# Optimization experiments

Hardware: AMD Instinct MI355X
Metric: run time of the kernel (lower is better)

## Reference

```python
import jax, jax.numpy as jnp
import numpy as np

N = 100_000      # nodes
E = 1_600_000    # directed edges
D_IN, D_H, D_OUT = 128, 128, 1


def setup_inputs() -> dict:
    key = jax.random.key(0)
    ks = jax.random.split(key, 6)
    x = jax.random.normal(ks[0], (N, D_IN), dtype=jnp.float32)
    edge_index = jax.random.randint(ks[1], (2, E), 0, N, dtype=jnp.int32)
    # GCNConv params (glorot-ish scale)
    W1 = jax.random.normal(ks[2], (D_IN, D_H), dtype=jnp.float32) / np.sqrt(D_IN)
    b1 = jnp.zeros((D_H,), dtype=jnp.float32)
    W2 = jax.random.normal(ks[3], (D_H, D_OUT), dtype=jnp.float32) / np.sqrt(D_H)
    b2 = jnp.zeros((D_OUT,), dtype=jnp.float32)
    return {"x": x, "edge_index": edge_index, "W1": W1, "b1": b1, "W2": W2, "b2": b2}


def _gcn_layer(x, src, dst, norm, W, b):
    # PyG GCNConv: linear transform, then sym-normalized neighbor sum (self-loops included in src/dst)
    h = x @ W                                  # [N, d_out]
    msg = h[src] * norm[:, None]               # [E+N, d_out] gather + scale
    out = jax.ops.segment_sum(msg, dst, num_segments=N)  # scatter-add
    return out + b


def reference(x, edge_index, W1, b1, W2, b2):
    loops = jnp.arange(N, dtype=edge_index.dtype)
    src = jnp.concatenate([edge_index[0], loops])  # [E+N]
    dst = jnp.concatenate([edge_index[1], loops])
    # symmetric normalization D^{-1/2} (A+I) D^{-1/2}
    deg = jax.ops.segment_sum(jnp.ones_like(dst, dtype=x.dtype), dst, num_segments=N)
    dis = jnp.where(deg > 0, jax.lax.rsqrt(deg), 0.0)
    norm = dis[src] * dis[dst]
    h = jax.nn.relu(_gcn_layer(x, src, dst, norm, W1, b1))
    return _gcn_layer(h, src, dst, norm, W2, b2)
```

## Files before the change

### kernel.cpp

```cpp
#include <hip/hip_runtime.h>
#include <hip/hip_fp16.h>

#define D 128
#define BSHIFT 9
#define MAXB 512
#define CHUNK 8192
#define CAP 12288
#define GP 8
#define OSTR 144

#define QS   (6.5f / 127.f)
#define QSI  (127.f / 6.5f)
#define WSC  (QS / 8192.f)

typedef _Float16 f16x8 __attribute__((ext_vector_type(8)));
typedef float f32x4 __attribute__((ext_vector_type(4)));

__global__ __launch_bounds__(512) void bin_k(const int* __restrict__ src,
                                             const int* __restrict__ dst,
                                             int* __restrict__ bcur,
                                             unsigned int* __restrict__ pairs,
                                             const float* __restrict__ W1,
                                             _Float16* __restrict__ w1t,
                                             unsigned char* __restrict__ h1s8,
                                             int E, int N) {
    __shared__ int h[MAXB];
    __shared__ int cur[MAXB];
    const int t = threadIdx.x;

    if (blockIdx.x == gridDim.x - 1) {
#pragma unroll
        for (int u = 0; u < 32; ++u) {
            int idx = u * 512 + t;
            int k = idx >> 7, n = idx & 127;
            w1t[n * 128 + k] = (_Float16)W1[idx];
        }
        if (t < 8) {
            int4 z = {0, 0, 0, 0};
            ((int4*)(h1s8 + (size_t)N * 128))[t] = z;
        }
    }

    if (t < MAXB) h[t] = 0;
    __syncthreads();
    const int base = blockIdx.x * CHUNK;
    int s_[16], d_[16];
    int n = 0;
#pragma unroll
    for (int u = 0; u < 16; ++u) {
        int e = base + u * 512 + t;
        if (e < E) {
            s_[u] = src[e];
            d_[u] = dst[e];
            atomicAdd(&h[d_[u] >> BSHIFT], 1);
            n = u + 1;
        }
    }
    __syncthreads();
    if (t < MAXB) {
        int i = t;
        cur[i] = h[i] ? (i * CAP + atomicAdd(&bcur[i], h[i])) : 0;
    }
    __syncthreads();
#pragma unroll
    for (int u = 0; u < 16; ++u) {
        if (u < n) {
            int b = d_[u] >> BSHIFT;
            int pos = atomicAdd(&cur[b], 1);
            if (pos - b * CAP < CAP)
                pairs[pos] = ((unsigned int)(d_[u] & ((1 << BSHIFT) - 1)) << 23) |
                             (unsigned int)s_[u];
        }
    }
}

__global__ __launch_bounds__(512) void csrA_k(const unsigned int* __restrict__ pairs,
                                              const int* __restrict__ bcur,
                                              int* __restrict__ offs,
                                              int* __restrict__ deg,
                                              float* __restrict__ dis,
                                              int* __restrict__ btotal,
                                              float* __restrict__ g, int N) {
    __shared__ int hist[512];
    __shared__ int scan[512];
    const int b = blockIdx.x;
    const int t = threadIdx.x;
    const int vb = b << BSHIFT;
    const int ebeg = b * CAP;
    int cnt = bcur[b]; cnt = cnt < CAP ? cnt : CAP;
    const int eend = ebeg + cnt;

    if (b == 0 && t == 0) g[N] = 0.f;

    hist[t] = 0;
    __syncthreads();
    for (int e = ebeg + t; e < eend; e += 512)
        atomicAdd(&hist[pairs[e] >> 23], 1);
    __syncthreads();

    const int c = hist[t];
    const int p8 = (c + 7) & ~7;
    scan[t] = p8;
    __syncthreads();
    for (int o = 1; o < 512; o <<= 1) {
        int a = (t >= o) ? scan[t - o] : 0;
        __syncthreads();
        scan[t] += a;
        __syncthreads();
    }

    int v = vb + t;
    if (v < N) {
        offs[v] = ebeg + scan[t] - p8;
        deg[v] = c;
        dis[v] = rsqrtf((float)(c + 1));
    }
    if (t == 511) btotal[b] = scan[511];
}

__global__ __launch_bounds__(512) void csrB_k(const unsigned int* __restrict__ pairs,
                                              const int* __restrict__ bcur,
                                              const int* __restrict__ offs,
                                              const float* __restrict__ dis,
                                              const int* __restrict__ btotal,
                                              int* __restrict__ edge_src, int N) {
    __shared__ int cur[512];
    __shared__ int buf[CAP];
    const int b = blockIdx.x;
    const int t = threadIdx.x;
    const int vb = b << BSHIFT;
    const int ebeg = b * CAP;
    int cnt = bcur[b]; cnt = cnt < CAP ? cnt : CAP;
    const int eend = ebeg + cnt;
    const int total = btotal[b];

    for (int j = t; j < total; j += 512) buf[j] = N;
    {
        int v = vb + t;
        cur[t] = (v < N) ? (offs[v] - ebeg) : 0;
    }
    __syncthreads();

    for (int e = ebeg + t; e < eend; e += 512) {
        unsigned int p = pairs[e];
        int s = (int)(p & 0x7FFFFFu);
        int q = (int)rintf(dis[s] * 8192.f);
        int pos = atomicAdd(&cur[p >> 23], 1);
        buf[pos] = (q << 17) | s;
    }
    __syncthreads();

    const int n4 = total >> 2;
    for (int j = t; j < n4; j += 512)
        ((int4*)(edge_src + ebeg))[j] = ((const int4*)buf)[j];
}


__global__ __launch_bounds__(256) void gemm_k(const float* __restrict__ x,
                                              const _Float16* __restrict__ w1t,
                                              unsigned char* __restrict__ h1s8, int N) {
    __shared__ _Float16 xs[128][128 + GP];
    __shared__ _Float16 ws[128][128 + GP];

    const int tid = threadIdx.x;
    const int row0 = blockIdx.x * 128;

#pragma unroll
    for (int u = 0; u < 16; ++u) {
        int f = u * 256 + tid;
        int r = f >> 5, c4 = f & 31;
        int rg = row0 + r; rg = rg < N ? rg : N - 1;
        float4 v = ((const float4*)(x + (size_t)rg * D))[c4];
        union { _Float16 h[4]; uint2 u2; } tmp;
        tmp.h[0] = (_Float16)v.x; tmp.h[1] = (_Float16)v.y;
        tmp.h[2] = (_Float16)v.z; tmp.h[3] = (_Float16)v.w;
        *(uint2*)&xs[r][c4 * 4] = tmp.u2;
    }
#pragma unroll
    for (int u = 0; u < 8; ++u) {
        int f = u * 256 + tid;
        int r = f >> 4, c8 = f & 15;
        int4 v = ((const int4*)(w1t + r * 128))[c8];
        *(int4*)&ws[r][c8 * 8] = v;
    }
    __syncthreads();

    const int wave = tid >> 6, lane = tid & 63;
    const int qr = lane & 15;
    const int quad = lane >> 4;
    const int m0 = wave * 32;

    f32x4 acc[2][8] = {};
#pragma unroll
    for (int kt = 0; kt < 4; ++kt) {
        const int kk = kt * 32 + quad * 8;
        f16x8 a0 = *(const f16x8*)&xs[m0 + qr][kk];
        f16x8 a1 = *(const f16x8*)&xs[m0 + 16 + qr][kk];
#pragma unroll
        for (int n = 0; n < 8; ++n) {
            f16x8 b = *(const f16x8*)&ws[n * 16 + qr][kk];
            acc[0][n] = __builtin_amdgcn_mfma_f32_16x16x32_f16(a0, b, acc[0][n], 0, 0, 0);
            acc[1][n] = __builtin_amdgcn_mfma_f32_16x16x32_f16(a1, b, acc[1][n], 0, 0, 0);
        }
    }

    __syncthreads();
    unsigned char* os = (unsigned char*)&ws[0][0];
#pragma unroll
    for (int mt = 0; mt < 2; ++mt)
#pragma unroll
        for (int n = 0; n < 8; ++n)
#pragma unroll
            for (int r = 0; r < 4; ++r) {
                int row = m0 + mt * 16 + quad * 4 + r;
                float qf = fminf(fmaxf(acc[mt][n][r] * QSI, -127.f), 127.f);
                int q = (int)rintf(qf);
                os[row * OSTR + n * 16 + qr] = (unsigned char)(q & 0xFF);
            }
    __syncthreads();

#pragma unroll
    for (int u = 0; u < 4; ++u) {
        int f = u * 256 + tid;
        int r = f >> 3, c16 = f & 7;
        int rg = row0 + r;
        if (rg < N)
            ((int4*)(h1s8 + (size_t)rg * 128))[c16] = *(const int4*)(os + r * OSTR + c16 * 16);
    }
}


__device__ __forceinline__ void accw(float* aq, int Wd, float wt) {
    aq[0] = fmaf(wt, (float)((Wd << 24) >> 24), aq[0]);
    aq[1] = fmaf(wt, (float)((Wd << 16) >> 24), aq[1]);
    aq[2] = fmaf(wt, (float)((Wd <<  8) >> 24), aq[2]);
    aq[3] = fmaf(wt, (float)( Wd        >> 24), aq[3]);
}
__device__ __forceinline__ void accr(float* a, const int4& rr, float wt) {
    accw(a +  0, rr.x, wt);
    accw(a +  4, rr.y, wt);
    accw(a +  8, rr.z, wt);
    accw(a + 12, rr.w, wt);
}


__global__ __launch_bounds__(256) void agg1_k(const unsigned char* __restrict__ h1s8,
                                              const int* __restrict__ edge_src,
                                              const int* __restrict__ offs,
                                              const int* __restrict__ deg,
                                              const float* __restrict__ dis,
                                              const float* __restrict__ b1,
                                              const float* __restrict__ W2,
                                              float* __restrict__ g, int N) {
    const int c = threadIdx.x & 7;
    const int v = blockIdx.x * 32 + (threadIdx.x >> 3);
    if (v >= N) return;

    const float dv = dis[v];
    float a[16] = {};
    {
        int4 sv = *(const int4*)(h1s8 + (size_t)v * 128 + c * 16);
        accr(a, sv, dv * QS);
    }

    const int beg = offs[v];
    const int p8 = (deg[v] + 7) & ~7;
    const int4* ip = (const int4*)(edge_src + beg);
    int4 s0 = ip[0], s1 = ip[1];

    for (int i = 0; i < p8; i += 8) {
        int4 n0 = ip[2], n1 = ip[3];
        int i0 = s0.x & 0x1FFFF, i1 = s0.y & 0x1FFFF;
        int i2 = s0.z & 0x1FFFF, i3 = s0.w & 0x1FFFF;
        int i4 = s1.x & 0x1FFFF, i5 = s1.y & 0x1FFFF;
        int i6 = s1.z & 0x1FFFF, i7 = s1.w & 0x1FFFF;
        float w0 = (float)((unsigned)s0.x >> 17) * WSC;
        float w1 = (float)((unsigned)s0.y >> 17) * WSC;
        float w2 = (float)((unsigned)s0.z >> 17) * WSC;
        float w3 = (float)((unsigned)s0.w >> 17) * WSC;
        float w4 = (float)((unsigned)s1.x >> 17) * WSC;
        float w5 = (float)((unsigned)s1.y >> 17) * WSC;
        float w6 = (float)((unsigned)s1.z >> 17) * WSC;
        float w7 = (float)((unsigned)s1.w >> 17) * WSC;
        int4 r0 = *(const int4*)(h1s8 + (size_t)i0 * 128 + c * 16);
        int4 r1 = *(const int4*)(h1s8 + (size_t)i1 * 128 + c * 16);
        int4 r2 = *(const int4*)(h1s8 + (size_t)i2 * 128 + c * 16);
        int4 r3 = *(const int4*)(h1s8 + (size_t)i3 * 128 + c * 16);
        int4 r4 = *(const int4*)(h1s8 + (size_t)i4 * 128 + c * 16);
        int4 r5 = *(const int4*)(h1s8 + (size_t)i5 * 128 + c * 16);
        int4 r6 = *(const int4*)(h1s8 + (size_t)i6 * 128 + c * 16);
        int4 r7 = *(const int4*)(h1s8 + (size_t)i7 * 128 + c * 16);
        accr(a, r0, w0); accr(a, r1, w1); accr(a, r2, w2); accr(a, r3, w3);
        accr(a, r4, w4); accr(a, r5, w5); accr(a, r6, w6); accr(a, r7, w7);
        s0 = n0; s1 = n1; ip += 2;
    }

    float p = 0.f;
#pragma unroll
    for (int q4 = 0; q4 < 4; ++q4) {
        float4 bb = ((const float4*)b1)[c * 4 + q4];
        float4 ww = ((const float4*)W2)[c * 4 + q4];
        p += fmaxf(fmaf(dv, a[q4 * 4 + 0], bb.x), 0.f) * ww.x
           + fmaxf(fmaf(dv, a[q4 * 4 + 1], bb.y), 0.f) * ww.y
           + fmaxf(fmaf(dv, a[q4 * 4 + 2], bb.z), 0.f) * ww.z
           + fmaxf(fmaf(dv, a[q4 * 4 + 3], bb.w), 0.f) * ww.w;
    }
#pragma unroll
    for (int o = 4; o >= 1; o >>= 1) p += __shfl_xor(p, o, 64);
    if (c == 0) g[v] = dv * p;
}


__global__ void agg2_k(const float* __restrict__ g, const int* __restrict__ edge_src,
                       const int* __restrict__ offs, const int* __restrict__ deg,
                       const float* __restrict__ dis, const float* __restrict__ b2,
                       float* __restrict__ out, int N) {
    int v = blockIdx.x * 256 + threadIdx.x;
    if (v >= N) return;
    float acc = g[v];
    const int beg = offs[v];
    const int p8 = (deg[v] + 7) & ~7;
    const int4* ip = (const int4*)(edge_src + beg);
    int4 s0 = ip[0], s1 = ip[1];
    for (int i = 0; i < p8; i += 8) {
        int4 n0 = ip[2], n1 = ip[3];
        acc += (g[s0.x & 0x1FFFF] + g[s0.y & 0x1FFFF])
             + (g[s0.z & 0x1FFFF] + g[s0.w & 0x1FFFF])
             + (g[s1.x & 0x1FFFF] + g[s1.y & 0x1FFFF])
             + (g[s1.z & 0x1FFFF] + g[s1.w & 0x1FFFF]);
        s0 = n0; s1 = n1; ip += 2;
    }
    out[v] = fmaf(dis[v], acc, b2[0]);
}


extern "C" void kernel_launch(void* const* d_in, const int* in_sizes, int n_in,
                              void* d_out, int out_size, void* d_ws, size_t ws_size,
                              hipStream_t stream) {
    const float* x  = (const float*)d_in[0];
    const int*   ei = (const int*)d_in[1];
    const float* W1 = (const float*)d_in[2];
    const float* b1 = (const float*)d_in[3];
    const float* W2 = (const float*)d_in[4];
    const float* b2 = (const float*)d_in[5];
    float* out = (float*)d_out;

    const int N = in_sizes[0] / D;
    const int E = in_sizes[1] / 2;
    const int* srcp = ei;
    const int* dstp = ei + E;
    const int nbuck = (N + (1 << BSHIFT) - 1) >> BSHIFT;
    const int nbin  = (E + CHUNK - 1) / CHUNK;

    char* p = (char*)d_ws;
    auto alloc = [&](size_t bytes) {
        void* q = (void*)p;
        p += (bytes + 255) & ~(size_t)255;
        return q;
    };
    unsigned char* h1s8     = (unsigned char*)alloc((size_t)(N + 1) * 128);
    float*         g        = (float*)alloc((size_t)(N + 1) * sizeof(float));
    float*         dis      = (float*)alloc((size_t)(N + 1) * sizeof(float));
    int*           offs     = (int*)alloc((size_t)N * sizeof(int));
    int*           deg      = (int*)alloc((size_t)N * sizeof(int));
    int*           edge_src = (int*)alloc(((size_t)nbuck * CAP + 64) * sizeof(int));
    unsigned int*  pairs    = (unsigned int*)alloc((size_t)nbuck * CAP * sizeof(unsigned int));
    _Float16*      w1t      = (_Float16*)alloc((size_t)D * D * sizeof(_Float16));
    int*           btotal   = (int*)alloc((size_t)nbuck * sizeof(int));
    int*           bcur     = (int*)alloc(MAXB * sizeof(int));

    const int nb = (N + 255) / 256;

    hipMemsetAsync(bcur, 0, MAXB * sizeof(int), stream);
    bin_k<<<nbin, 512, 0, stream>>>(srcp, dstp, bcur, pairs, W1, w1t, h1s8, E, N);
    csrA_k<<<nbuck, 512, 0, stream>>>(pairs, bcur, offs, deg, dis, btotal, g, N);
    csrB_k<<<nbuck, 512, 0, stream>>>(pairs, bcur, offs, dis, btotal, edge_src, N);
    gemm_k<<<(N + 127) / 128, 256, 0, stream>>>(x, w1t, h1s8, N);
    agg1_k<<<(N + 31) / 32, 256, 0, stream>>>(h1s8, edge_src, offs, deg, dis, b1, W2, g, N);
    agg2_k<<<nb, 256, 0, stream>>>(g, edge_src, offs, deg, dis, b2, out, N);
}
```

Before: 184.3 us.

## Stage binned edge pairs in LDS and write them out bucket-contiguously

The binning kernel now computes a block-local prefix scan over bucket counts, places each packed pair into a shared-memory buffer ordered by bucket, and then writes the buffer out with consecutive threads mapping to consecutive global positions within each bucket. The aim is to turn the scattered per-edge global stores into mostly coalesced runs. In exchange it uses about 48KB of extra LDS per block, which can lower occupancy, and adds a 9-step scan with barriers.

Result: no change. 185.8 us (+0.8%).

```diff
diff --git a/kernel.cpp b/kernel.cpp
--- a/kernel.cpp
+++ b/kernel.cpp
@@ -25,7 +25,11 @@
                                              unsigned char* __restrict__ h1s8,
                                              int E, int N) {
     __shared__ int h[MAXB];
-    __shared__ int cur[MAXB];
+    __shared__ int scn[MAXB];
+    __shared__ int gbase[MAXB];
+    __shared__ int lcur[MAXB];
+    __shared__ unsigned int buf[CHUNK];
+    __shared__ unsigned short bid[CHUNK];
     const int t = threadIdx.x;
 
     if (blockIdx.x == gridDim.x - 1) {
@@ -41,9 +45,10 @@
         }
     }
 
-    if (t < MAXB) h[t] = 0;
+    h[t] = 0;
     __syncthreads();
     const int base = blockIdx.x * CHUNK;
+    const int cnt = (E - base) < CHUNK ? (E - base) : CHUNK;
     int s_[16], d_[16];
     int n = 0;
 #pragma unroll
@@ -57,20 +62,33 @@
         }
     }
     __syncthreads();
-    if (t < MAXB) {
-        int i = t;
-        cur[i] = h[i] ? (i * CAP + atomicAdd(&bcur[i], h[i])) : 0;
-    }
+    gbase[t] = h[t] ? (t * CAP + atomicAdd(&bcur[t], h[t])) : 0;
+    scn[t] = h[t];
+    __syncthreads();
+    for (int o = 1; o < 512; o <<= 1) {
+        int a = (t >= o) ? scn[t - o] : 0;
+        __syncthreads();
+        scn[t] += a;
+        __syncthreads();
+    }
+    lcur[t] = scn[t] - h[t];
     __syncthreads();
 #pragma unroll
     for (int u = 0; u < 16; ++u) {
         if (u < n) {
             int b = d_[u] >> BSHIFT;
-            int pos = atomicAdd(&cur[b], 1);
-            if (pos - b * CAP < CAP)
-                pairs[pos] = ((unsigned int)(d_[u] & ((1 << BSHIFT) - 1)) << 23) |
-                             (unsigned int)s_[u];
-        }
+            int p = atomicAdd(&lcur[b], 1);
+            buf[p] = ((unsigned int)(d_[u] & ((1 << BSHIFT) - 1)) << 23) |
+                     (unsigned int)s_[u];
+            bid[p] = (unsigned short)b;
+        }
+    }
+    __syncthreads();
+    for (int j = t; j < cnt; j += 512) {
+        int b = bid[j];
+        int pos = gbase[b] + (j - (scn[b] - h[b]));
+        if (pos - b * CAP < CAP)
+            pairs[pos] = buf[j];
     }
 }
 
```

## Fuse edge binning and layer-1 GEMM into one interleaved kernel launch

Applied to the files above, without the earlier changes.

Merges the edge-binning kernel and the x@W1 GEMM kernel into a single launch. Blocks with index divisible by 5 do binning and the rest do 128-row GEMM tiles, so the two independent phases overlap on the GPU. Each GEMM block now transposes and converts W1 to fp16 into shared memory itself, which removes the separate w1t buffer and the dependency on it. The cost is redundant W1 loads and uncoalesced LDS transpose writes in every GEMM block, a 512-thread block with larger shared memory that may limit occupancy, and GEMM work that now sits in front of the CSR kernels.

New measurement: 188.3 us. +2.2%, slower.

```diff
diff --git a/kernel.cpp b/kernel.cpp
--- a/kernel.cpp
+++ b/kernel.cpp
@@ -16,61 +16,123 @@
 typedef _Float16 f16x8 __attribute__((ext_vector_type(8)));
 typedef float f32x4 __attribute__((ext_vector_type(4)));
 
-__global__ __launch_bounds__(512) void bin_k(const int* __restrict__ src,
-                                             const int* __restrict__ dst,
-                                             int* __restrict__ bcur,
-                                             unsigned int* __restrict__ pairs,
-                                             const float* __restrict__ W1,
-                                             _Float16* __restrict__ w1t,
-                                             unsigned char* __restrict__ h1s8,
-                                             int E, int N) {
-    __shared__ int h[MAXB];
-    __shared__ int cur[MAXB];
+__global__ __launch_bounds__(512) void fused_k(const int* __restrict__ src,
+                                               const int* __restrict__ dst,
+                                               int* __restrict__ bcur,
+                                               unsigned int* __restrict__ pairs,
+                                               const float* __restrict__ x,
+                                               const float* __restrict__ W1,
+                                               unsigned char* __restrict__ h1s8,
+                                               int E, int N, int nbin, int ngemm) {
+    __shared__ union {
+        struct { int h[MAXB]; int cur[MAXB]; } b;
+        struct { _Float16 xs[128][128 + GP]; _Float16 ws[128][128 + GP]; } g;
+    } S;
     const int t = threadIdx.x;
-
-    if (blockIdx.x == gridDim.x - 1) {
-#pragma unroll
-        for (int u = 0; u < 32; ++u) {
-            int idx = u * 512 + t;
-            int k = idx >> 7, n = idx & 127;
-            w1t[n * 128 + k] = (_Float16)W1[idx];
-        }
-        if (t < 8) {
+    const int bid = blockIdx.x;
+
+    if (bid % 5 == 0) {
+        const int bb = bid / 5;
+        if (bb >= nbin) return;
+        if (bb == 0 && t < 8) {
             int4 z = {0, 0, 0, 0};
             ((int4*)(h1s8 + (size_t)N * 128))[t] = z;
         }
-    }
-
-    if (t < MAXB) h[t] = 0;
-    __syncthreads();
-    const int base = blockIdx.x * CHUNK;
-    int s_[16], d_[16];
-    int n = 0;
-#pragma unroll
-    for (int u = 0; u < 16; ++u) {
-        int e = base + u * 512 + t;
-        if (e < E) {
-            s_[u] = src[e];
-            d_[u] = dst[e];
-            atomicAdd(&h[d_[u] >> BSHIFT], 1);
-            n = u + 1;
-        }
-    }
-    __syncthreads();
-    if (t < MAXB) {
-        int i = t;
-        cur[i] = h[i] ? (i * CAP + atomicAdd(&bcur[i], h[i])) : 0;
-    }
-    __syncthreads();
-#pragma unroll
-    for (int u = 0; u < 16; ++u) {
-        if (u < n) {
-            int b = d_[u] >> BSHIFT;
-            int pos = atomicAdd(&cur[b], 1);
-            if (pos - b * CAP < CAP)
-                pairs[pos] = ((unsigned int)(d_[u] & ((1 << BSHIFT) - 1)) << 23) |
-                             (unsigned int)s_[u];
-        }
+        S.b.h[t] = 0;
+        __syncthreads();
+        const int base = bb * CHUNK;
+        int s_[16], d_[16];
+        int n = 0;
+#pragma unroll
+        for (int u = 0; u < 16; ++u) {
+            int e = base + u * 512 + t;
+            if (e < E) {
+                s_[u] = src[e];
+                d_[u] = dst[e];
+                atomicAdd(&S.b.h[d_[u] >> BSHIFT], 1);
+                n = u + 1;
+            }
+        }
+        __syncthreads();
+        S.b.cur[t] = S.b.h[t] ? (t * CAP + atomicAdd(&bcur[t], S.b.h[t])) : 0;
+        __syncthreads();
+#pragma unroll
+        for (int u = 0; u < 16; ++u) {
+            if (u < n) {
+                int b = d_[u] >> BSHIFT;
+                int pos = atomicAdd(&S.b.cur[b], 1);
+                if (pos - b * CAP < CAP)
+                    pairs[pos] = ((unsigned int)(d_[u] & ((1 << BSHIFT) - 1)) << 23) |
+                                 (unsigned int)s_[u];
+            }
+        }
+        return;
+    }
+
+    const int gb = bid - bid / 5 - 1;
+    if (gb >= ngemm) return;
+    const int row0 = gb * 128;
+
+#pragma unroll
+    for (int u = 0; u < 8; ++u) {
+        int f = u * 512 + t;
+        int r = f >> 5, c4 = f & 31;
+        int rg = row0 + r; rg = rg < N ? rg : N - 1;
+        float4 v = ((const float4*)(x + (size_t)rg * D))[c4];
+        union { _Float16 h[4]; uint2 u2; } tmp;
+        tmp.h[0] = (_Float16)v.x; tmp.h[1] = (_Float16)v.y;
+        tmp.h[2] = (_Float16)v.z; tmp.h[3] = (_Float16)v.w;
+        *(uint2*)&S.g.xs[r][c4 * 4] = tmp.u2;
+    }
+#pragma unroll
+    for (int u = 0; u < 8; ++u) {
+        int f = u * 512 + t;
+        int k = f >> 5, n4 = f & 31;
+        float4 w = ((const float4*)(W1 + (size_t)k * 128))[n4];
+        S.g.ws[n4 * 4 + 0][k] = (_Float16)w.x;
+        S.g.ws[n4 * 4 + 1][k] = (_Float16)w.y;
+        S.g.ws[n4 * 4 + 2][k] = (_Float16)w.z;
+        S.g.ws[n4 * 4 + 3][k] = (_Float16)w.w;
+    }
+    __syncthreads();
+
+    const int wave = t >> 6, lane = t & 63;
+    const int qr = lane & 15;
+    const int quad = lane >> 4;
+    const int m0 = wave * 16;
+
+    f32x4 acc[8] = {};
+#pragma unroll
+    for (int kt = 0; kt < 4; ++kt) {
+        const int kk = kt * 32 + quad * 8;
+        f16x8 a0 = *(const f16x8*)&S.g.xs[m0 + qr][kk];
+#pragma unroll
+        for (int n = 0; n < 8; ++n) {
+            f16x8 b = *(const f16x8*)&S.g.ws[n * 16 + qr][kk];
+            acc[n] = __builtin_amdgcn_mfma_f32_16x16x32_f16(a0, b, acc[n], 0, 0, 0);
+        }
+    }
+
+    __syncthreads();
+    unsigned char* os = (unsigned char*)&S.g.ws[0][0];
+#pragma unroll
+    for (int n = 0; n < 8; ++n)
+#pragma unroll
+        for (int r = 0; r < 4; ++r) {
+            int row = m0 + quad * 4 + r;
+            float qf = fminf(fmaxf(acc[n][r] * QSI, -127.f), 127.f);
+            int q = (int)rintf(qf);
+            os[row * OSTR + n * 16 + qr] = (unsigned char)(q & 0xFF);
+        }
+    __syncthreads();
+
+#pragma unroll
+    for (int u = 0; u < 2; ++u) {
+        int f = u * 512 + t;
+        int r = f >> 3, c16 = f & 7;
+        int rg = row0 + r;
+        if (rg < N)
+            ((int4*)(h1s8 + (size_t)rg * 128))[c16] = *(const int4*)(os + r * OSTR + c16 * 16);
     }
 }
 
@@ -153,80 +215,6 @@
     const int n4 = total >> 2;
     for (int j = t; j < n4; j += 512)
         ((int4*)(edge_src + ebeg))[j] = ((const int4*)buf)[j];
-}
-
-
-__global__ __launch_bounds__(256) void gemm_k(const float* __restrict__ x,
-                                              const _Float16* __restrict__ w1t,
-                                              unsigned char* __restrict__ h1s8, int N) {
-    __shared__ _Float16 xs[128][128 + GP];
-    __shared__ _Float16 ws[128][128 + GP];
-
-    const int tid = threadIdx.x;
-    const int row0 = blockIdx.x * 128;
-
-#pragma unroll
-    for (int u = 0; u < 16; ++u) {
-        int f = u * 256 + tid;
-        int r = f >> 5, c4 = f & 31;
-        int rg = row0 + r; rg = rg < N ? rg : N - 1;
-        float4 v = ((const float4*)(x + (size_t)rg * D))[c4];
-        union { _Float16 h[4]; uint2 u2; } tmp;
-        tmp.h[0] = (_Float16)v.x; tmp.h[1] = (_Float16)v.y;
-        tmp.h[2] = (_Float16)v.z; tmp.h[3] = (_Float16)v.w;
-        *(uint2*)&xs[r][c4 * 4] = tmp.u2;
-    }
-#pragma unroll
-    for (int u = 0; u < 8; ++u) {
-        int f = u * 256 + tid;
-        int r = f >> 4, c8 = f & 15;
-        int4 v = ((const int4*)(w1t + r * 128))[c8];
-        *(int4*)&ws[r][c8 * 8] = v;
-    }
-    __syncthreads();
-
-    const int wave = tid >> 6, lane = tid & 63;
-    const int qr = lane & 15;
-    const int quad = lane >> 4;
-    const int m0 = wave * 32;
-
-    f32x4 acc[2][8] = {};
-#pragma unroll
-    for (int kt = 0; kt < 4; ++kt) {
-        const int kk = kt * 32 + quad * 8;
-        f16x8 a0 = *(const f16x8*)&xs[m0 + qr][kk];
-        f16x8 a1 = *(const f16x8*)&xs[m0 + 16 + qr][kk];
-#pragma unroll
-        for (int n = 0; n < 8; ++n) {
-            f16x8 b = *(const f16x8*)&ws[n * 16 + qr][kk];
-            acc[0][n] = __builtin_amdgcn_mfma_f32_16x16x32_f16(a0, b, acc[0][n], 0, 0, 0);
-            acc[1][n] = __builtin_amdgcn_mfma_f32_16x16x32_f16(a1, b, acc[1][n], 0, 0, 0);
-        }
-    }
-
-    __syncthreads();
-    unsigned char* os = (unsigned char*)&ws[0][0];
-#pragma unroll
-    for (int mt = 0; mt < 2; ++mt)
-#pragma unroll
-        for (int n = 0; n < 8; ++n)
-#pragma unroll
-            for (int r = 0; r < 4; ++r) {
-                int row = m0 + mt * 16 + quad * 4 + r;
-                float qf = fminf(fmaxf(acc[mt][n][r] * QSI, -127.f), 127.f);
-                int q = (int)rintf(qf);
-                os[row * OSTR + n * 16 + qr] = (unsigned char)(q & 0xFF);
-            }
-    __syncthreads();
-
-#pragma unroll
-    for (int u = 0; u < 4; ++u) {
-        int f = u * 256 + tid;
-        int r = f >> 3, c16 = f & 7;
-        int rg = row0 + r;
-        if (rg < N)
-            ((int4*)(h1s8 + (size_t)rg * 128))[c16] = *(const int4*)(os + r * OSTR + c16 * 16);
-    }
 }
 
 
@@ -351,6 +339,9 @@
     const int* dstp = ei + E;
     const int nbuck = (N + (1 << BSHIFT) - 1) >> BSHIFT;
     const int nbin  = (E + CHUNK - 1) / CHUNK;
+    const int ngemm = (N + 127) / 128;
+    int NG = 5 * nbin;
+    if (NG - (NG + 4) / 5 < ngemm) NG = ngemm + nbin + 8;
 
     char* p = (char*)d_ws;
     auto alloc = [&](size_t bytes) {
@@ -365,17 +356,16 @@
     int*           deg      = (int*)alloc((size_t)N * sizeof(int));
     int*           edge_src = (int*)alloc(((size_t)nbuck * CAP + 64) * sizeof(int));
     unsigned int*  pairs    = (unsigned int*)alloc((size_t)nbuck * CAP * sizeof(unsigned int));
-    _Float16*      w1t      = (_Float16*)alloc((size_t)D * D * sizeof(_Float16));
     int*           btotal   = (int*)alloc((size_t)nbuck * sizeof(int));
     int*           bcur     = (int*)alloc(MAXB * sizeof(int));
 
     const int nb = (N + 255) / 256;
 
     hipMemsetAsync(bcur, 0, MAXB * sizeof(int), stream);
-    bin_k<<<nbin, 512, 0, stream>>>(srcp, dstp, bcur, pairs, W1, w1t, h1s8, E, N);
+    fused_k<<<NG, 512, 0, stream>>>(srcp, dstp, bcur, pairs, x, W1, h1s8,
+                                    E, N, nbin, ngemm);
     csrA_k<<<nbuck, 512, 0, stream>>>(pairs, bcur, offs, deg, dis, btotal, g, N);
     csrB_k<<<nbuck, 512, 0, stream>>>(pairs, bcur, offs, dis, btotal, edge_src, N);
-    gemm_k<<<(N + 127) / 128, 256, 0, stream>>>(x, w1t, h1s8, N);
     agg1_k<<<(N + 31) / 32, 256, 0, stream>>>(h1s8, edge_src, offs, deg, dis, b1, W2, g, N);
     agg2_k<<<nb, 256, 0, stream>>>(g, edge_src, offs, deg, dis, b2, out, N);
 }
```
